# Performance work log

Measured on AMD Instinct MI355X. Metric: run time of the kernel, lower is better.

## Reference

```python
import jax, jax.numpy as jnp
import numpy as np

P_DROP = 0.1
KEEP = 1.0 - P_DROP


def setup_inputs() -> dict:
    key = jax.random.key(0)
    ks = jax.random.split(key, 8)
    N, E, D, H, O, L = 50000, 800000, 128, 128, 64, 3
    x = jax.random.normal(ks[0], (N, D), dtype=jnp.float32)
    edge_index = jax.random.randint(ks[1], (2, E), 0, N, dtype=jnp.int64)
    s = 0.05  # weight scale for numeric stability
    Ws1 = jax.random.normal(ks[2], (L, D, H), dtype=jnp.float32) * s
    bs1 = jnp.zeros((L, H), dtype=jnp.float32)
    Ws2 = jax.random.normal(ks[3], (L, H, H), dtype=jnp.float32) * s
    bs2 = jnp.zeros((L, H), dtype=jnp.float32)
    Wlin = jax.random.normal(ks[4], (H, O), dtype=jnp.float32) * s
    blin = jnp.zeros((O,), dtype=jnp.float32)
    return {"x": x, "edge_index": edge_index, "Ws1": Ws1, "bs1": bs1,
            "Ws2": Ws2, "bs2": bs2, "Wlin": Wlin, "blin": blin}


def _gin_conv(x, src, dst, W1, b1, W2, b2, n_nodes):
    # GINConv (eps=0): h = MLP(x + sum_{j in N(i)} x_j)
    agg = jax.ops.segment_sum(x[src], dst, num_segments=n_nodes)  # [N, D]
    h = x + agg
    h = jax.nn.relu(h @ W1 + b1)
    h = jax.nn.relu(h @ W2 + b2)
    return h


def reference(x, edge_index, Ws1, bs1, Ws2, bs2, Wlin, blin):
    n_nodes = x.shape[0]
    src, dst = edge_index[0], edge_index[1]  # PyG flow: message from src to dst
    L = Ws1.shape[0]
    dkeys = jax.random.split(jax.random.key(42), L)
    h = x
    for l in range(L):
        h = _gin_conv(h, src, dst, Ws1[l], bs1[l], Ws2[l], bs2[l], n_nodes)
        h = jax.nn.relu(h)
        mask = jax.random.bernoulli(dkeys[l], KEEP, h.shape)
        h = jnp.where(mask, h / KEEP, 0.0)  # dropout p=0.1, training=True
    return h @ Wlin + blin
```

## Files before the change

kernel.cpp:

```cpp
#include <hip/hip_runtime.h>
#include <stdint.h>

typedef short short8 __attribute__((ext_vector_type(8)));
typedef float float4v __attribute__((ext_vector_type(4)));

#define SLOTS 24

__device__ static inline unsigned short f2bf(float f) {
  uint32_t u = __float_as_uint(f);
  u += 0x7fffu + ((u >> 16) & 1u);
  return (unsigned short)(u >> 16);
}
__device__ static inline float bf_lo(uint32_t v) { return __uint_as_float(v << 16); }
__device__ static inline float bf_hi(uint32_t v) { return __uint_as_float(v & 0xffff0000u); }

__host__ __device__ static inline void tf2x32(uint32_t k0, uint32_t k1,
                                              uint32_t x0, uint32_t x1,
                                              uint32_t* o0, uint32_t* o1) {
  const uint32_t ks2 = k0 ^ k1 ^ 0x1BD11BDAu;
  x0 += k0; x1 += k1;
#define TF_RND(r) { x0 += x1; x1 = (x1 << (r)) | (x1 >> (32 - (r))); x1 ^= x0; }
  TF_RND(13) TF_RND(15) TF_RND(26) TF_RND(6)
  x0 += k1;  x1 += ks2 + 1u;
  TF_RND(17) TF_RND(29) TF_RND(16) TF_RND(24)
  x0 += ks2; x1 += k0 + 2u;
  TF_RND(13) TF_RND(15) TF_RND(26) TF_RND(6)
  x0 += k0;  x1 += k1 + 3u;
  TF_RND(17) TF_RND(29) TF_RND(16) TF_RND(24)
  x0 += k1;  x1 += ks2 + 4u;
  TF_RND(13) TF_RND(15) TF_RND(26) TF_RND(6)
  x0 += ks2; x1 += k0 + 5u;
#undef TF_RND
  *o0 = x0; *o1 = x1;
}

__device__ static inline bool tf_keep(uint32_t k0, uint32_t k1, uint32_t idx) {
  uint32_t o0, o1;
  tf2x32(k0, k1, 0u, idx, &o0, &o1);
  const uint32_t bits = o0 ^ o1;
  const float u = __uint_as_float((bits >> 9) | 0x3f800000u) - 1.0f;
  return u < 0.9f;
}

__device__ static inline uint32_t mask_word(uint32_t k0, uint32_t k1, int b, int t) {
  const int wave = t >> 6, lane = t & 63;
  const int ch = wave & 1, rtw = wave >> 1;
  const int m = lane & 15, kg = lane >> 4;
  const int node0 = b * 64;
  uint32_t km = 0;
#pragma unroll
  for (int rt = 0; rt < 2; ++rt) {
#pragma unroll
    for (int nt = 0; nt < 4; ++nt) {
      const int col = ch * 64 + nt * 16 + m;
#pragma unroll
      for (int r = 0; r < 4; ++r) {
        const int ro = node0 + (rtw * 2 + rt) * 16 + kg * 4 + r;
        if (tf_keep(k0, k1, (uint32_t)ro * 128u + (uint32_t)col))
          km |= 1u << (rt * 16 + nt * 4 + r);
      }
    }
  }
  return km;
}

__global__ __launch_bounds__(256) void build_kernel(
    const int* __restrict__ src, const int* __restrict__ dst,
    int* __restrict__ cnt8, unsigned short* __restrict__ slots, int N, int E,
    const float* __restrict__ x, unsigned short* __restrict__ xb,
    unsigned short* __restrict__ xb2, int n4,
    const float* __restrict__ Ws1, const float* __restrict__ Ws2,
    const float* __restrict__ Wlin, unsigned short* __restrict__ wpack,
    int nFill, int nConv, int nPer) {
  const int t = threadIdx.x;
  const int g = blockIdx.x;
  if (g < 72 * nPer) {
    const int m = g / 72, s = g % 72;
    if (s < 8) {
      const int j = m * 8 + s;
      if (j >= nFill) return;
      const int tid = j * 256 + t;
      const int nt4 = (E + 3) >> 2;
      if (tid >= nt4) return;
      const size_t segbase = (size_t)(j & 7) * N;
      const int base = tid * 4;
      if (base + 4 <= E) {
        const int4 s4 = ((const int4*)src)[tid];
        const int4 d4 = ((const int4*)dst)[tid];
        const int p0 = atomicAdd(&cnt8[segbase + d4.x], 1);
        const int p1 = atomicAdd(&cnt8[segbase + d4.y], 1);
        const int p2 = atomicAdd(&cnt8[segbase + d4.z], 1);
        const int p3 = atomicAdd(&cnt8[segbase + d4.w], 1);
        if (p0 < SLOTS) slots[(segbase + d4.x) * SLOTS + p0] = (unsigned short)s4.x;
        if (p1 < SLOTS) slots[(segbase + d4.y) * SLOTS + p1] = (unsigned short)s4.y;
        if (p2 < SLOTS) slots[(segbase + d4.z) * SLOTS + p2] = (unsigned short)s4.z;
        if (p3 < SLOTS) slots[(segbase + d4.w) * SLOTS + p3] = (unsigned short)s4.w;
      } else {
        for (int k = base; k < E; ++k) {
          const int d = dst[k];
          const int p = atomicAdd(&cnt8[segbase + d], 1);
          if (p < SLOTS) slots[(segbase + d) * SLOTS + p] = (unsigned short)src[k];
        }
      }
      return;
    }
    const int c = m * 64 + (s - 8);
    if (c >= nConv) return;
    const int i = c * 256 + t;
    if (i < n4) {
      const float4 v = ((const float4*)x)[i];
      uint2 o;
      o.x = (uint32_t)f2bf(v.x) | ((uint32_t)f2bf(v.y) << 16);
      o.y = (uint32_t)f2bf(v.z) | ((uint32_t)f2bf(v.w) << 16);
      ((uint2*)xb)[i] = o;
    } else if (i < n4 + 32) {
      uint2 z; z.x = 0u; z.y = 0u;
      ((uint2*)xb)[i] = z;
      ((uint2*)xb2)[i] = z;
    }
    return;
  }
  const int tid = (g - 72 * nPer) * 256 + t;
  if (tid >= 13312) return;
  const float* W;
  int cols, r;
  size_t obase;
  if (tid < 12288) {
    const int mm = tid / 2048;
    r = tid % 2048;
    const int l = mm >> 1;
    W = (mm & 1) ? (Ws2 + (size_t)l * 16384) : (Ws1 + (size_t)l * 16384);
    cols = 128;
    obase = (size_t)mm * 16384;
  } else {
    r = tid - 12288;
    W = Wlin;
    cols = 64;
    obase = 6 * 16384;
  }
  const int ch = (cols == 128) ? (r >> 10) : 0;
  const int kt = (r >> 8) & 3;
  const int nt = (r >> 6) & 3;
  const int lane = r & 63;
  const int n = ch * 64 + nt * 16 + (lane & 15);
  const int kbase = kt * 32 + (lane >> 4) * 8;
  unsigned short o[8];
#pragma unroll
  for (int j = 0; j < 8; ++j) o[j] = f2bf(W[(size_t)(kbase + j) * cols + n]);
  uint4 ov;
  ov.x = (uint32_t)o[0] | ((uint32_t)o[1] << 16);
  ov.y = (uint32_t)o[2] | ((uint32_t)o[3] << 16);
  ov.z = (uint32_t)o[4] | ((uint32_t)o[5] << 16);
  ov.w = (uint32_t)o[6] | ((uint32_t)o[7] << 16);
  *(uint4*)(wpack + obase + ((size_t)((ch * 16 + kt * 4 + nt) * 64 + lane)) * 8) = ov;
}

#define ACC16(vv, A0,A1,A2,A3,A4,A5,A6,A7)                         \
  A0 += bf_lo(vv.x); A1 += bf_hi(vv.x); A2 += bf_lo(vv.y); A3 += bf_hi(vv.y); \
  A4 += bf_lo(vv.z); A5 += bf_hi(vv.z); A6 += bf_lo(vv.w); A7 += bf_hi(vv.w);

template <bool LAST>
__global__ __launch_bounds__(256, 3) void gin_layer_kernel(
    const unsigned short* __restrict__ hIn, unsigned short* __restrict__ hOut,
    const unsigned short* __restrict__ slots, const int* __restrict__ cnt8,
    const unsigned short* __restrict__ W1p, const float* __restrict__ b1,
    const unsigned short* __restrict__ W2p, const float* __restrict__ b2,
    const unsigned short* __restrict__ WLp, const float* __restrict__ bL,
    float* __restrict__ outF,
    uint32_t dk0, uint32_t dk1, int N) {
  __shared__ __align__(16) unsigned short agg[64 * 136];
  __shared__ __align__(16) unsigned short t1[64 * 136];
  const int t = threadIdx.x;
  const int q = t & 15;
  const int gb = (t & 63) & 48;
  const int node0 = blockIdx.x * 64;
  const uint4* hv = (const uint4*)hIn;
  const int NS = N * SLOTS;

  for (int p = 0; p < 4; ++p) {
    const int nn = p * 16 + (t >> 4);
    const int node = node0 + nn;
    if (node < N) {
      int ol = 0;
      if (q < 8) {
        ol = cnt8[(size_t)q * N + node];
        ol = (ol < SLOTS) ? ol : SLOTS;
      }
      const int l0 = __shfl(ol, gb + 0, 64);
      const int l1 = __shfl(ol, gb + 1, 64);
      const int l2 = __shfl(ol, gb + 2, 64);
      const int l3 = __shfl(ol, gb + 3, 64);
      const int l4 = __shfl(ol, gb + 4, 64);
      const int l5 = __shfl(ol, gb + 5, 64);
      const int l6 = __shfl(ol, gb + 6, 64);
      const int l7 = __shfl(ol, gb + 7, 64);
      const int c1 = l0, c2 = c1 + l1, c3 = c2 + l2, c4 = c3 + l3;
      const int c5 = c4 + l4, c6 = c5 + l5, c7 = c6 + l6, T = c7 + l7;
      const int nb = node * SLOTS;
      const int sb0 = nb;
      const int sb1 = 1 * NS + nb - c1;
      const int sb2 = 2 * NS + nb - c2;
      const int sb3 = 3 * NS + nb - c3;
      const int sb4 = 4 * NS + nb - c4;
      const int sb5 = 5 * NS + nb - c5;
      const int sb6 = 6 * NS + nb - c6;
      const int sb7 = 7 * NS + nb - c7;

      const uint4 sv = hv[(size_t)node * 16 + q];
      float a0 = bf_lo(sv.x), a1 = bf_hi(sv.x), a2 = bf_lo(sv.y), a3 = bf_hi(sv.y);
      float a4 = bf_lo(sv.z), a5 = bf_hi(sv.z), a6 = bf_lo(sv.w), a7 = bf_hi(sv.w);
      float d0 = 0.f, d1 = 0.f, d2 = 0.f, d3 = 0.f, d4 = 0.f, d5 = 0.f, d6 = 0.f, d7 = 0.f;

      for (int base = 0; base < T; base += 16) {
        const int j = base + q;
        int pos = sb0 + j;
        pos = (j >= c1) ? (sb1 + j) : pos;
        pos = (j >= c2) ? (sb2 + j) : pos;
        pos = (j >= c3) ? (sb3 + j) : pos;
        pos = (j >= c4) ? (sb4 + j) : pos;
        pos = (j >= c5) ? (sb5 + j) : pos;
        pos = (j >= c6) ? (sb6 + j) : pos;
        pos = (j >= c7) ? (sb7 + j) : pos;
        const int idx = (j < T) ? (int)slots[pos] : N;
        uint4 v[16];
#pragma unroll
        for (int jj = 0; jj < 16; ++jj) {
          const int s = __shfl(idx, gb + jj, 64);
          v[jj] = hv[(size_t)s * 16 + q];
        }
#pragma unroll
        for (int jj = 0; jj < 16; jj += 2) {
          ACC16(v[jj], a0, a1, a2, a3, a4, a5, a6, a7)
          ACC16(v[jj + 1], d0, d1, d2, d3, d4, d5, d6, d7)
        }
      }
      a0 += d0; a1 += d1; a2 += d2; a3 += d3;
      a4 += d4; a5 += d5; a6 += d6; a7 += d7;

      uint4 ov;
      ov.x = (uint32_t)f2bf(a0) | ((uint32_t)f2bf(a1) << 16);
      ov.y = (uint32_t)f2bf(a2) | ((uint32_t)f2bf(a3) << 16);
      ov.z = (uint32_t)f2bf(a4) | ((uint32_t)f2bf(a5) << 16);
      ov.w = (uint32_t)f2bf(a6) | ((uint32_t)f2bf(a7) << 16);
      *(uint4*)(agg + (size_t)nn * 136 + q * 8) = ov;
    }
  }
  const uint32_t km = mask_word(dk0, dk1, blockIdx.x, t);
  __syncthreads();

  const int wave = t >> 6, lane = t & 63;
  const int ch = wave & 1;
  const int rtw = wave >> 1;
  const int m = lane & 15, kg = lane >> 4;

  short8 bfrag[16];
  {
    const short8* wp = (const short8*)W1p + (size_t)(ch * 16) * 64 + lane;
#pragma unroll
    for (int i = 0; i < 16; ++i) bfrag[i] = wp[(size_t)i * 64];
  }
  float4v acc[2][4] = {};
#pragma unroll
  for (int rt = 0; rt < 2; ++rt) {
    const int lrow = (rtw * 2 + rt) * 16 + m;
#pragma unroll
    for (int kt = 0; kt < 4; ++kt) {
      const short8 af = *(const short8*)(agg + (size_t)lrow * 136 + kt * 32 + kg * 8);
#pragma unroll
      for (int nt = 0; nt < 4; ++nt)
        acc[rt][nt] = __builtin_amdgcn_mfma_f32_16x16x32_bf16(
            af, bfrag[kt * 4 + nt], acc[rt][nt], 0, 0, 0);
    }
  }
#pragma unroll
  for (int rt = 0; rt < 2; ++rt) {
#pragma unroll
    for (int nt = 0; nt < 4; ++nt) {
      const int col = ch * 64 + nt * 16 + m;
      const float bb = b1[col];
#pragma unroll
      for (int r = 0; r < 4; ++r) {
        const int lrow = (rtw * 2 + rt) * 16 + kg * 4 + r;
        float v = acc[rt][nt][r] + bb;
        v = fmaxf(v, 0.0f);
        t1[(size_t)lrow * 136 + col] = f2bf(v);
      }
    }
  }
  __syncthreads();

  {
    const short8* wp = (const short8*)W2p + (size_t)(ch * 16) * 64 + lane;
#pragma unroll
    for (int i = 0; i < 16; ++i) bfrag[i] = wp[(size_t)i * 64];
  }
  float4v acc2[2][4] = {};
#pragma unroll
  for (int rt = 0; rt < 2; ++rt) {
    const int lrow = (rtw * 2 + rt) * 16 + m;
#pragma unroll
    for (int kt = 0; kt < 4; ++kt) {
      const short8 af = *(const short8*)(t1 + (size_t)lrow * 136 + kt * 32 + kg * 8);
#pragma unroll
      for (int nt = 0; nt < 4; ++nt)
        acc2[rt][nt] = __builtin_amdgcn_mfma_f32_16x16x32_bf16(
            af, bfrag[kt * 4 + nt], acc2[rt][nt], 0, 0, 0);
    }
  }
  const float KEEP_INV = 1.0f / 0.9f;
#pragma unroll
  for (int rt = 0; rt < 2; ++rt) {
#pragma unroll
    for (int nt = 0; nt < 4; ++nt) {
      const int col = ch * 64 + nt * 16 + m;
      const float bb = b2[col];
#pragma unroll
      for (int r = 0; r < 4; ++r) {
        const int lrow = (rtw * 2 + rt) * 16 + kg * 4 + r;
        float v = acc2[rt][nt][r] + bb;
        v = fmaxf(v, 0.0f);
        v = ((km >> (rt * 16 + nt * 4 + r)) & 1u) ? v * KEEP_INV : 0.0f;
        agg[(size_t)lrow * 136 + col] = f2bf(v);
      }
    }
  }
  __syncthreads();

  if (!LAST) {
    const int orow = t >> 2;
    const int oc0 = (t & 3) * 8;
    const int gnode = node0 + orow;
    if (gnode < N) {
#pragma unroll
      for (int i = 0; i < 4; ++i) {
        const uint4 vv = *(const uint4*)(agg + (size_t)orow * 136 + oc0 + i * 32);
        *(uint4*)(hOut + (size_t)gnode * 128 + oc0 + i * 32) = vv;
      }
    }
  } else {
    short8 wfrag[16];
    {
      const short8* wp = (const short8*)WLp + lane;
#pragma unroll
      for (int i = 0; i < 16; ++i) wfrag[i] = wp[(size_t)i * 64];
    }
    float4v acc3[4] = {};
#pragma unroll
    for (int kt = 0; kt < 4; ++kt) {
      const short8 af = *(const short8*)(agg + (size_t)(wave * 16 + m) * 136 + kt * 32 + kg * 8);
#pragma unroll
      for (int nt = 0; nt < 4; ++nt)
        acc3[nt] = __builtin_amdgcn_mfma_f32_16x16x32_bf16(
            af, wfrag[kt * 4 + nt], acc3[nt], 0, 0, 0);
    }
#pragma unroll
    for (int nt = 0; nt < 4; ++nt) {
      const int col = nt * 16 + m;
      const float bb = bL[col];
#pragma unroll
      for (int r = 0; r < 4; ++r) {
        const int ro = node0 + wave * 16 + kg * 4 + r;
        if (ro < N) outF[(size_t)ro * 64 + col] = acc3[nt][r] + bb;
      }
    }
  }
}

extern "C" void kernel_launch(void* const* d_in, const int* in_sizes, int n_in,
                              void* d_out, int out_size, void* d_ws, size_t ws_size,
                              hipStream_t stream) {
  const float* x    = (const float*)d_in[0];
  const int*   ei   = (const int*)d_in[1];
  const float* Ws1  = (const float*)d_in[2];
  const float* bs1  = (const float*)d_in[3];
  const float* Ws2  = (const float*)d_in[4];
  const float* bs2  = (const float*)d_in[5];
  const float* Wlin = (const float*)d_in[6];
  const float* blin = (const float*)d_in[7];

  const int N = in_sizes[0] / 128;
  const int E = in_sizes[1] / 2;
  const int* src = ei;
  const int* dst = ei + E;
  const int M8 = 8 * N;
  const int lblocks = (N + 63) / 64;

  unsigned short* bufA  = (unsigned short*)d_ws;
  unsigned short* bufB  = bufA + (size_t)(N + 1) * 128;
  unsigned short* wpack = bufB + (size_t)(N + 1) * 128;
  int* cnt8 = (int*)(wpack + 106512);
  unsigned short* slots = (unsigned short*)(cnt8 + M8);

  uint32_t dk[3][2];
  for (int l = 0; l < 3; ++l)
    tf2x32(0u, 42u, 0u, (uint32_t)l, &dk[l][0], &dk[l][1]);

  const int nt4 = (E + 3) / 4;
  const int eblocks = (nt4 + 255) / 256;
  const int nconv = (N * 32 + 32 + 255) / 256;

  int P = (eblocks + 7) / 8;
  if ((nconv + 63) / 64 > P) P = (nconv + 63) / 64;
  const int build_grid = 72 * P + 52;

  hipMemsetAsync(cnt8, 0, (size_t)M8 * sizeof(int), stream);
  build_kernel<<<build_grid, 256, 0, stream>>>(
      src, dst, cnt8, slots, N, E,
      x, bufA, bufB, N * 32, Ws1, Ws2, Wlin, wpack,
      eblocks, nconv, P);

  gin_layer_kernel<false><<<lblocks, 256, 0, stream>>>(
      bufA, bufB, slots, cnt8,
      wpack + 0 * 16384, bs1 + 0, wpack + 1 * 16384, bs2 + 0,
      nullptr, nullptr, nullptr, dk[0][0], dk[0][1], N);
  gin_layer_kernel<false><<<lblocks, 256, 0, stream>>>(
      bufB, bufA, slots, cnt8,
      wpack + 2 * 16384, bs1 + 128, wpack + 3 * 16384, bs2 + 128,
      nullptr, nullptr, nullptr, dk[1][0], dk[1][1], N);
  gin_layer_kernel<true><<<lblocks, 256, 0, stream>>>(
      bufA, nullptr, slots, cnt8,
      wpack + 4 * 16384, bs1 + 256, wpack + 5 * 16384, bs2 + 256,
      wpack + 6 * 16384, blin, (float*)d_out,
      dk[2][0], dk[2][1], N);
}
```

Before: 290.7 us.

## Shrink GIN layer tile to 32 nodes per block for higher occupancy

Each layer block now handles 32 nodes instead of 64, which halves the LDS buffers and each wave's MFMA accumulators and dropout-mask work. The launch-bounds occupancy hint rises from 3 to 6 blocks per CU and the grid doubles. The goal is more waves in flight to hide latency in the gather-heavy aggregation phase. In exchange, every block reloads the full W1/W2 fragments for half as many rows, and the final linear and output-copy indexing are remapped to the new tile.

```diff
diff --git a/kernel.cpp b/kernel.cpp
--- a/kernel.cpp
+++ b/kernel.cpp
@@ -40,28 +40,6 @@
   const uint32_t bits = o0 ^ o1;
   const float u = __uint_as_float((bits >> 9) | 0x3f800000u) - 1.0f;
   return u < 0.9f;
-}
-
-__device__ static inline uint32_t mask_word(uint32_t k0, uint32_t k1, int b, int t) {
-  const int wave = t >> 6, lane = t & 63;
-  const int ch = wave & 1, rtw = wave >> 1;
-  const int m = lane & 15, kg = lane >> 4;
-  const int node0 = b * 64;
-  uint32_t km = 0;
-#pragma unroll
-  for (int rt = 0; rt < 2; ++rt) {
-#pragma unroll
-    for (int nt = 0; nt < 4; ++nt) {
-      const int col = ch * 64 + nt * 16 + m;
-#pragma unroll
-      for (int r = 0; r < 4; ++r) {
-        const int ro = node0 + (rtw * 2 + rt) * 16 + kg * 4 + r;
-        if (tf_keep(k0, k1, (uint32_t)ro * 128u + (uint32_t)col))
-          km |= 1u << (rt * 16 + nt * 4 + r);
-      }
-    }
-  }
-  return km;
 }
 
 __global__ __launch_bounds__(256) void build_kernel(
@@ -160,7 +138,7 @@
   A4 += bf_lo(vv.z); A5 += bf_hi(vv.z); A6 += bf_lo(vv.w); A7 += bf_hi(vv.w);
 
 template <bool LAST>
-__global__ __launch_bounds__(256, 3) void gin_layer_kernel(
+__global__ __launch_bounds__(256, 6) void gin_layer_kernel(
     const unsigned short* __restrict__ hIn, unsigned short* __restrict__ hOut,
     const unsigned short* __restrict__ slots, const int* __restrict__ cnt8,
     const unsigned short* __restrict__ W1p, const float* __restrict__ b1,
@@ -168,16 +146,16 @@
     const unsigned short* __restrict__ WLp, const float* __restrict__ bL,
     float* __restrict__ outF,
     uint32_t dk0, uint32_t dk1, int N) {
-  __shared__ __align__(16) unsigned short agg[64 * 136];
-  __shared__ __align__(16) unsigned short t1[64 * 136];
+  __shared__ __align__(16) unsigned short agg[32 * 136];
+  __shared__ __align__(16) unsigned short t1[32 * 136];
   const int t = threadIdx.x;
   const int q = t & 15;
   const int gb = (t & 63) & 48;
-  const int node0 = blockIdx.x * 64;
+  const int node0 = blockIdx.x * 32;
   const uint4* hv = (const uint4*)hIn;
   const int NS = N * SLOTS;
 
-  for (int p = 0; p < 4; ++p) {
+  for (int p = 0; p < 2; ++p) {
     const int nn = p * 16 + (t >> 4);
     const int node = node0 + nn;
     if (node < N) {
@@ -245,13 +223,22 @@
       *(uint4*)(agg + (size_t)nn * 136 + q * 8) = ov;
     }
   }
-  const uint32_t km = mask_word(dk0, dk1, blockIdx.x, t);
-  __syncthreads();
-
   const int wave = t >> 6, lane = t & 63;
   const int ch = wave & 1;
-  const int rtw = wave >> 1;
+  const int rt = wave >> 1;
   const int m = lane & 15, kg = lane >> 4;
+  uint32_t km = 0;
+#pragma unroll
+  for (int nt = 0; nt < 4; ++nt) {
+    const int col = ch * 64 + nt * 16 + m;
+#pragma unroll
+    for (int r = 0; r < 4; ++r) {
+      const int ro = node0 + rt * 16 + kg * 4 + r;
+      if (tf_keep(dk0, dk1, (uint32_t)ro * 128u + (uint32_t)col))
+        km |= 1u << (nt * 4 + r);
+    }
+  }
+  __syncthreads();
 
   short8 bfrag[16];
   {
@@ -259,32 +246,28 @@
 #pragma unroll
     for (int i = 0; i < 16; ++i) bfrag[i] = wp[(size_t)i * 64];
   }
-  float4v acc[2][4] = {};
-#pragma unroll
-  for (int rt = 0; rt < 2; ++rt) {
-    const int lrow = (rtw * 2 + rt) * 16 + m;
+  float4v acc[4] = {};
+  {
+    const int lrowA = rt * 16 + m;
 #pragma unroll
     for (int kt = 0; kt < 4; ++kt) {
-      const short8 af = *(const short8*)(agg + (size_t)lrow * 136 + kt * 32 + kg * 8);
+      const short8 af = *(const short8*)(agg + (size_t)lrowA * 136 + kt * 32 + kg * 8);
 #pragma unroll
       for (int nt = 0; nt < 4; ++nt)
-        acc[rt][nt] = __builtin_amdgcn_mfma_f32_16x16x32_bf16(
-            af, bfrag[kt * 4 + nt], acc[rt][nt], 0, 0, 0);
-    }
-  }
-#pragma unroll
-  for (int rt = 0; rt < 2; ++rt) {
-#pragma unroll
-    for (int nt = 0; nt < 4; ++nt) {
-      const int col = ch * 64 + nt * 16 + m;
-      const float bb = b1[col];
-#pragma unroll
-      for (int r = 0; r < 4; ++r) {
-        const int lrow = (rtw * 2 + rt) * 16 + kg * 4 + r;
-        float v = acc[rt][nt][r] + bb;
-        v = fmaxf(v, 0.0f);
-        t1[(size_t)lrow * 136 + col] = f2bf(v);
-      }
+        acc[nt] = __builtin_amdgcn_mfma_f32_16x16x32_bf16(
+            af, bfrag[kt * 4 + nt], acc[nt], 0, 0, 0);
+    }
+  }
+#pragma unroll
+  for (int nt = 0; nt < 4; ++nt) {
+    const int col = ch * 64 + nt * 16 + m;
+    const float bb = b1[col];
+#pragma unroll
+    for (int r = 0; r < 4; ++r) {
+      const int lrow = rt * 16 + kg * 4 + r;
+      float v = acc[nt][r] + bb;
+      v = fmaxf(v, 0.0f);
+      t1[(size_t)lrow * 136 + col] = f2bf(v);
     }
   }
   __syncthreads();
@@ -294,73 +277,72 @@
 #pragma unroll
     for (int i = 0; i < 16; ++i) bfrag[i] = wp[(size_t)i * 64];
   }
-  float4v acc2[2][4] = {};
-#pragma unroll
-  for (int rt = 0; rt < 2; ++rt) {
-    const int lrow = (rtw * 2 + rt) * 16 + m;
+  float4v acc2[4] = {};
+  {
+    const int lrowA = rt * 16 + m;
 #pragma unroll
     for (int kt = 0; kt < 4; ++kt) {
-      const short8 af = *(const short8*)(t1 + (size_t)lrow * 136 + kt * 32 + kg * 8);
+      const short8 af = *(const short8*)(t1 + (size_t)lrowA * 136 + kt * 32 + kg * 8);
 #pragma unroll
       for (int nt = 0; nt < 4; ++nt)
-        acc2[rt][nt] = __builtin_amdgcn_mfma_f32_16x16x32_bf16(
-            af, bfrag[kt * 4 + nt], acc2[rt][nt], 0, 0, 0);
+        acc2[nt] = __builtin_amdgcn_mfma_f32_16x16x32_bf16(
+            af, bfrag[kt * 4 + nt], acc2[nt], 0, 0, 0);
     }
   }
   const float KEEP_INV = 1.0f / 0.9f;
 #pragma unroll
-  for (int rt = 0; rt < 2; ++rt) {
-#pragma unroll
-    for (int nt = 0; nt < 4; ++nt) {
-      const int col = ch * 64 + nt * 16 + m;
-      const float bb = b2[col];
-#pragma unroll
-      for (int r = 0; r < 4; ++r) {
-        const int lrow = (rtw * 2 + rt) * 16 + kg * 4 + r;
-        float v = acc2[rt][nt][r] + bb;
-        v = fmaxf(v, 0.0f);
-        v = ((km >> (rt * 16 + nt * 4 + r)) & 1u) ? v * KEEP_INV : 0.0f;
-        agg[(size_t)lrow * 136 + col] = f2bf(v);
-      }
+  for (int nt = 0; nt < 4; ++nt) {
+    const int col = ch * 64 + nt * 16 + m;
+    const float bb = b2[col];
+#pragma unroll
+    for (int r = 0; r < 4; ++r) {
+      const int lrow = rt * 16 + kg * 4 + r;
+      float v = acc2[nt][r] + bb;
+      v = fmaxf(v, 0.0f);
+      v = ((km >> (nt * 4 + r)) & 1u) ? v * KEEP_INV : 0.0f;
+      agg[(size_t)lrow * 136 + col] = f2bf(v);
     }
   }
   __syncthreads();
 
   if (!LAST) {
-    const int orow = t >> 2;
-    const int oc0 = (t & 3) * 8;
+    const int orow = t >> 3;
+    const int oc0 = (t & 7) * 16;
     const int gnode = node0 + orow;
     if (gnode < N) {
 #pragma unroll
-      for (int i = 0; i < 4; ++i) {
-        const uint4 vv = *(const uint4*)(agg + (size_t)orow * 136 + oc0 + i * 32);
-        *(uint4*)(hOut + (size_t)gnode * 128 + oc0 + i * 32) = vv;
+      for (int i = 0; i < 2; ++i) {
+        const uint4 vv = *(const uint4*)(agg + (size_t)orow * 136 + oc0 + i * 8);
+        *(uint4*)(hOut + (size_t)gnode * 128 + oc0 + i * 8) = vv;
       }
     }
   } else {
-    short8 wfrag[16];
+    short8 wfrag[8];
     {
-      const short8* wp = (const short8*)WLp + lane;
-#pragma unroll
-      for (int i = 0; i < 16; ++i) wfrag[i] = wp[(size_t)i * 64];
-    }
-    float4v acc3[4] = {};
+#pragma unroll
+      for (int kt = 0; kt < 4; ++kt)
+#pragma unroll
+        for (int i = 0; i < 2; ++i)
+          wfrag[kt * 2 + i] =
+              ((const short8*)WLp)[(size_t)((kt * 4 + ch * 2 + i) * 64 + lane)];
+    }
+    float4v acc3[2] = {};
 #pragma unroll
     for (int kt = 0; kt < 4; ++kt) {
-      const short8 af = *(const short8*)(agg + (size_t)(wave * 16 + m) * 136 + kt * 32 + kg * 8);
-#pragma unroll
-      for (int nt = 0; nt < 4; ++nt)
-        acc3[nt] = __builtin_amdgcn_mfma_f32_16x16x32_bf16(
-            af, wfrag[kt * 4 + nt], acc3[nt], 0, 0, 0);
-    }
-#pragma unroll
-    for (int nt = 0; nt < 4; ++nt) {
-      const int col = nt * 16 + m;
+      const short8 af = *(const short8*)(agg + (size_t)(rt * 16 + m) * 136 + kt * 32 + kg * 8);
+#pragma unroll
+      for (int i = 0; i < 2; ++i)
+        acc3[i] = __builtin_amdgcn_mfma_f32_16x16x32_bf16(
+            af, wfrag[kt * 2 + i], acc3[i], 0, 0, 0);
+    }
+#pragma unroll
+    for (int i = 0; i < 2; ++i) {
+      const int col = (ch * 2 + i) * 16 + m;
       const float bb = bL[col];
 #pragma unroll
       for (int r = 0; r < 4; ++r) {
-        const int ro = node0 + wave * 16 + kg * 4 + r;
-        if (ro < N) outF[(size_t)ro * 64 + col] = acc3[nt][r] + bb;
+        const int ro = node0 + rt * 16 + kg * 4 + r;
+        if (ro < N) outF[(size_t)ro * 64 + col] = acc3[i][r] + bb;
       }
     }
   }
@@ -383,7 +365,7 @@
   const int* src = ei;
   const int* dst = ei + E;
   const int M8 = 8 * N;
-  const int lblocks = (N + 63) / 64;
+  const int lblocks = (N + 31) / 32;
 
   unsigned short* bufA  = (unsigned short*)d_ws;
   unsigned short* bufB  = bufA + (size_t)(N + 1) * 128;
```

After: 423.8 us. 1.46x slower.
